# Kernel optimization log

Hardware: AMD Instinct MI355X
Metric: run time of the kernel (lower is better)

Reference implementation:

```python
import jax, jax.numpy as jnp
import numpy as np

B, Q, C = 32, 900, 92
W_CLASS, W_BBOX, W_GIOU = 1.0, 1.0, 1.0
BIG = 100000000.0


def box_cxcywh_to_xyxy(b):
    cx, cy, w, h = b[..., 0], b[..., 1], b[..., 2], b[..., 3]
    return jnp.stack([cx - 0.5 * w, cy - 0.5 * h, cx + 0.5 * w, cy + 0.5 * h], axis=-1)


def pairwise_generalized_box_iou(b1, b2):
    # b1, b2: [B, Q, 4] in xyxy -> [B, Q, Q]
    area1 = (b1[..., 2] - b1[..., 0]) * (b1[..., 3] - b1[..., 1])  # [B,Q]
    area2 = (b2[..., 2] - b2[..., 0]) * (b2[..., 3] - b2[..., 1])  # [B,Q]
    lt = jnp.maximum(b1[:, :, None, :2], b2[:, None, :, :2])  # [B,Q,Q,2]
    rb = jnp.minimum(b1[:, :, None, 2:], b2[:, None, :, 2:])
    wh = jnp.clip(rb - lt, 0.0)
    inter = wh[..., 0] * wh[..., 1]  # [B,Q,Q]
    union = area1[:, :, None] + area2[:, None, :] - inter
    iou = inter / union
    # smallest enclosing box
    lt_e = jnp.minimum(b1[:, :, None, :2], b2[:, None, :, :2])
    rb_e = jnp.maximum(b1[:, :, None, 2:], b2[:, None, :, 2:])
    wh_e = jnp.clip(rb_e - lt_e, 0.0)
    enc = wh_e[..., 0] * wh_e[..., 1]
    return iou - (enc - union) / enc


def setup_inputs() -> dict:
    key = jax.random.key(0)
    k1, k2, k3, k4, k5 = jax.random.split(key, 5)
    return {
        "pred_logits": jax.random.normal(k1, (B, Q, C), dtype=jnp.float32),
        "pred_boxes": jax.random.uniform(k2, (B, Q, 4), dtype=jnp.float32),
        "boxes": jax.random.uniform(k3, (B, Q, 4), dtype=jnp.float32),
        "area": jax.random.uniform(k4, (B, Q), dtype=jnp.float32),
        "labels": jax.random.randint(k5, (B, Q), 0, C),
    }


def reference(pred_logits, pred_boxes, boxes, area, labels):
    b, q, _ = pred_logits.shape
    out_prob = jax.nn.softmax(pred_logits, axis=-1)  # [B,Q,C]
    # cost_class[b,i,j] = -out_prob[b,i,labels[b,j]]
    idx = jnp.broadcast_to(labels[:, None, :], (b, q, q))
    cost_class = -jnp.take_along_axis(out_prob, idx, axis=2)  # [B,Q,Q]
    # pairwise mean-L1 between cxcywh boxes (tf.reduce_mean over last dim)
    cost_bbox = jnp.mean(jnp.abs(pred_boxes[:, :, None, :] - boxes[:, None, :, :]), axis=-1)
    cost_giou = -pairwise_generalized_box_iou(
        box_cxcywh_to_xyxy(pred_boxes), box_cxcywh_to_xyxy(boxes)
    )
    cost = W_BBOX * cost_bbox + W_CLASS * cost_class + W_GIOU * cost_giou
    return jnp.where((area > 0)[:, None, :], cost, BIG)
```

## Files before the change

### kernel.cpp

```cpp
#include <hip/hip_runtime.h>
#include <math.h>

#define Bn  32
#define Qn  900
#define Cn  92
#define TI  12
#define NIT (Qn / TI)
#define NT  (Qn / 4)
#define BLK 256
#define BIGV 100000000.0f

__global__ __launch_bounds__(BLK) void hungarian_cost_kernel(
    const float* __restrict__ logits,
    const float* __restrict__ pboxes,
    const float* __restrict__ gboxes,
    const float* __restrict__ area,
    const int*   __restrict__ labels,
    float* __restrict__ out)
{
    __shared__ float s_x0[Qn], s_y0[Qn], s_x1[Qn], s_y1[Qn];
    __shared__ float s_ab[Qn];
    __shared__ float s_fl[Qn];
    __shared__ int   s_lab[Qn];
    __shared__ float s_prob[TI][Cn];
    __shared__ float4 s_pred[TI];
    __shared__ float  s_predA[TI];

    const int blk = blockIdx.x;
    const int b   = blk / NIT;
    const int i0  = (blk - b * NIT) * TI;
    const int tid = threadIdx.x;

    const float4* gb4 = (const float4*)(gboxes + (size_t)b * Qn * 4);
    const float*  ga  = area   + (size_t)b * Qn;
    const int*    gl  = labels + (size_t)b * Qn;
    for (int j = tid; j < Qn; j += BLK) {
        float4 c = gb4[j];
        s_x0[j] = c.x - 0.5f * c.z;
        s_y0[j] = c.y - 0.5f * c.w;
        s_x1[j] = c.x + 0.5f * c.z;
        s_y1[j] = c.y + 0.5f * c.w;
        s_ab[j] = c.z * c.w;
        s_fl[j] = (ga[j] > 0.0f) ? -3.402823e38f : BIGV;
        s_lab[j] = gl[j];
    }

    {
        const int wave = tid >> 6;
        const int lane = tid & 63;
        for (int rr = wave; rr < TI; rr += 4) {
            const int r = i0 + rr;
            const float* lrow = logits + ((size_t)(b * Qn + r)) * Cn;
            float x0 = lrow[lane];
            float x1 = (lane + 64 < Cn) ? lrow[lane + 64] : -INFINITY;
            float m = fmaxf(x0, x1);
            #pragma unroll
            for (int off = 32; off; off >>= 1)
                m = fmaxf(m, __shfl_xor(m, off));
            float e0 = __expf(x0 - m);
            float e1 = (lane + 64 < Cn) ? __expf(x1 - m) : 0.0f;
            float s = e0 + e1;
            #pragma unroll
            for (int off = 32; off; off >>= 1)
                s += __shfl_xor(s, off);
            float inv = __builtin_amdgcn_rcpf(s);
            s_prob[rr][lane] = e0 * inv;
            if (lane + 64 < Cn) s_prob[rr][lane + 64] = e1 * inv;
            if (lane == 0) {
                float4 c = ((const float4*)(pboxes + (size_t)b * Qn * 4))[r];
                float4 x;
                x.x = c.x - 0.5f * c.z;
                x.y = c.y - 0.5f * c.w;
                x.z = c.x + 0.5f * c.z;
                x.w = c.y + 0.5f * c.w;
                s_pred[rr]  = x;
                s_predA[rr] = c.z * c.w;
            }
        }
    }
    __syncthreads();

    float* obase = out + ((size_t)b * Qn + i0) * Qn;
    for (int f = tid; f < TI * NT; f += BLK) {
        const int il = f / NT;
        const int j4 = (f - il * NT) * 4;

        const float4 P     = s_pred[il];
        const float  areaP = s_predA[il];
        const float* prow  = s_prob[il];

        const float4 X0 = *(const float4*)&s_x0[j4];
        const float4 Y0 = *(const float4*)&s_y0[j4];
        const float4 X1 = *(const float4*)&s_x1[j4];
        const float4 Y1 = *(const float4*)&s_y1[j4];
        const float4 AB = *(const float4*)&s_ab[j4];
        const float4 FL = *(const float4*)&s_fl[j4];
        const int4   LB = *(const int4*)&s_lab[j4];

        auto cost1 = [&](float bx0, float by0, float bx1, float by1,
                         float ab, float fl, int lb) -> float {
            float dx0 = P.x - bx0, dy0 = P.y - by0;
            float dx1 = P.z - bx1, dy1 = P.w - by1;
            float s1 = fabsf(dx0 + dx1) + fabsf(dy0 + dy1);
            float s2 = fabsf(dx1 - dx0) + fabsf(dy1 - dy0);
            float bb = __builtin_fmaf(s1, 0.125f, 0.25f * s2);
            float iw = fminf(P.z, bx1) - fmaxf(P.x, bx0);
            float ih = fminf(P.w, by1) - fmaxf(P.y, by0);
            iw = fmaxf(iw, 0.0f); ih = fmaxf(ih, 0.0f);
            float inter = iw * ih;
            float uni = areaP + ab - inter;
            float ew = fmaxf(P.z, bx1) - fminf(P.x, bx0);
            float eh = fmaxf(P.w, by1) - fminf(P.y, by0);
            float enc = ew * eh;
            float rU = __builtin_amdgcn_rcpf(uni);
            float rE = __builtin_amdgcn_rcpf(enc);
            float g = __builtin_fmaf(inter, rU,
                      __builtin_fmaf(uni, rE, prow[lb] - 1.0f));
            float c = bb - g;
            return fmaxf(c, fl);
        };

        float4 res;
        res.x = cost1(X0.x, Y0.x, X1.x, Y1.x, AB.x, FL.x, LB.x);
        res.y = cost1(X0.y, Y0.y, X1.y, Y1.y, AB.y, FL.y, LB.y);
        res.z = cost1(X0.z, Y0.z, X1.z, Y1.z, AB.z, FL.z, LB.z);
        res.w = cost1(X0.w, Y0.w, X1.w, Y1.w, AB.w, FL.w, LB.w);

        ((float4*)(obase + (size_t)il * Qn))[j4 >> 2] = res;
    }
}

extern "C" void kernel_launch(void* const* d_in, const int* in_sizes, int n_in,
                              void* d_out, int out_size, void* d_ws, size_t ws_size,
                              hipStream_t stream) {
    const float* logits = (const float*)d_in[0];
    const float* pboxes = (const float*)d_in[1];
    const float* gboxes = (const float*)d_in[2];
    const float* areas  = (const float*)d_in[3];
    const int*   labels = (const int*)d_in[4];
    float* out = (float*)d_out;

    hungarian_cost_kernel<<<Bn * NIT, BLK, 0, stream>>>(
        logits, pboxes, gboxes, areas, labels, out);
}
```

Baseline: 45.32 us.

## Keep per-column GT box data in registers and use nontemporal output stores

Each thread now owns a fixed group of 4 target columns. It loads and transforms their boxes, areas and labels once into registers, instead of staging them in shared memory and re-reading them for every row. The per-row loop iterates over the 12 prediction rows with those registers reused, and writes results with nontemporal vector stores to avoid polluting the cache. Only 225 of 256 threads do output work, which slightly lowers lane utilization, and register pressure rises.

```diff
diff --git a/kernel.cpp b/kernel.cpp
--- a/kernel.cpp
+++ b/kernel.cpp
@@ -6,9 +6,12 @@
 #define Cn  92
 #define TI  12
 #define NIT (Qn / TI)
-#define NT  (Qn / 4)
+#define NG  (Qn / 4)
 #define BLK 256
 #define BIGV 100000000.0f
+#define NEGINF -3.402823e38f
+
+typedef float f32x4 __attribute__((ext_vector_type(4)));
 
 __global__ __launch_bounds__(BLK) void hungarian_cost_kernel(
     const float* __restrict__ logits,
@@ -18,11 +21,7 @@
     const int*   __restrict__ labels,
     float* __restrict__ out)
 {
-    __shared__ float s_x0[Qn], s_y0[Qn], s_x1[Qn], s_y1[Qn];
-    __shared__ float s_ab[Qn];
-    __shared__ float s_fl[Qn];
-    __shared__ int   s_lab[Qn];
-    __shared__ float s_prob[TI][Cn];
+    __shared__ float  s_prob[TI][Cn];
     __shared__ float4 s_pred[TI];
     __shared__ float  s_predA[TI];
 
@@ -31,25 +30,35 @@
     const int i0  = (blk - b * NIT) * TI;
     const int tid = threadIdx.x;
 
-    const float4* gb4 = (const float4*)(gboxes + (size_t)b * Qn * 4);
-    const float*  ga  = area   + (size_t)b * Qn;
-    const int*    gl  = labels + (size_t)b * Qn;
-    for (int j = tid; j < Qn; j += BLK) {
-        float4 c = gb4[j];
-        s_x0[j] = c.x - 0.5f * c.z;
-        s_y0[j] = c.y - 0.5f * c.w;
-        s_x1[j] = c.x + 0.5f * c.z;
-        s_y1[j] = c.y + 0.5f * c.w;
-        s_ab[j] = c.z * c.w;
-        s_fl[j] = (ga[j] > 0.0f) ? -3.402823e38f : BIGV;
-        s_lab[j] = gl[j];
+    float X0[4], Y0[4], X1[4], Y1[4], AB[4], FL[4];
+    int   LB[4];
+    if (tid < NG) {
+        const float4* gb4 = (const float4*)(gboxes + (size_t)b * Qn * 4) + tid * 4;
+        const float4  a4  = ((const float4*)(area   + (size_t)b * Qn))[tid];
+        const int4    l4  = ((const int4*)  (labels + (size_t)b * Qn))[tid];
+        #pragma unroll
+        for (int k = 0; k < 4; ++k) {
+            float4 c = gb4[k];
+            X0[k] = c.x - 0.5f * c.z;
+            Y0[k] = c.y - 0.5f * c.w;
+            X1[k] = c.x + 0.5f * c.z;
+            Y1[k] = c.y + 0.5f * c.w;
+            AB[k] = c.z * c.w;
+        }
+        FL[0] = (a4.x > 0.0f) ? NEGINF : BIGV;
+        FL[1] = (a4.y > 0.0f) ? NEGINF : BIGV;
+        FL[2] = (a4.z > 0.0f) ? NEGINF : BIGV;
+        FL[3] = (a4.w > 0.0f) ? NEGINF : BIGV;
+        LB[0] = l4.x; LB[1] = l4.y; LB[2] = l4.z; LB[3] = l4.w;
     }
 
     {
         const int wave = tid >> 6;
         const int lane = tid & 63;
-        for (int rr = wave; rr < TI; rr += 4) {
-            const int r = i0 + rr;
+        #pragma unroll
+        for (int rr0 = 0; rr0 < TI; rr0 += 4) {
+            const int rr = rr0 + wave;
+            const int r  = i0 + rr;
             const float* lrow = logits + ((size_t)(b * Qn + r)) * Cn;
             float x0 = lrow[lane];
             float x1 = (lane + 64 < Cn) ? lrow[lane + 64] : -INFINITY;
@@ -80,53 +89,38 @@
     }
     __syncthreads();
 
-    float* obase = out + ((size_t)b * Qn + i0) * Qn;
-    for (int f = tid; f < TI * NT; f += BLK) {
-        const int il = f / NT;
-        const int j4 = (f - il * NT) * 4;
+    if (tid < NG) {
+        float* obase = out + ((size_t)(b * Qn + i0)) * Qn + tid * 4;
+        for (int il = 0; il < TI; ++il) {
+            const float4 P     = s_pred[il];
+            const float  areaP = s_predA[il];
+            const float* prow  = s_prob[il];
 
-        const float4 P     = s_pred[il];
-        const float  areaP = s_predA[il];
-        const float* prow  = s_prob[il];
-
-        const float4 X0 = *(const float4*)&s_x0[j4];
-        const float4 Y0 = *(const float4*)&s_y0[j4];
-        const float4 X1 = *(const float4*)&s_x1[j4];
-        const float4 Y1 = *(const float4*)&s_y1[j4];
-        const float4 AB = *(const float4*)&s_ab[j4];
-        const float4 FL = *(const float4*)&s_fl[j4];
-        const int4   LB = *(const int4*)&s_lab[j4];
-
-        auto cost1 = [&](float bx0, float by0, float bx1, float by1,
-                         float ab, float fl, int lb) -> float {
-            float dx0 = P.x - bx0, dy0 = P.y - by0;
-            float dx1 = P.z - bx1, dy1 = P.w - by1;
-            float s1 = fabsf(dx0 + dx1) + fabsf(dy0 + dy1);
-            float s2 = fabsf(dx1 - dx0) + fabsf(dy1 - dy0);
-            float bb = __builtin_fmaf(s1, 0.125f, 0.25f * s2);
-            float iw = fminf(P.z, bx1) - fmaxf(P.x, bx0);
-            float ih = fminf(P.w, by1) - fmaxf(P.y, by0);
-            iw = fmaxf(iw, 0.0f); ih = fmaxf(ih, 0.0f);
-            float inter = iw * ih;
-            float uni = areaP + ab - inter;
-            float ew = fmaxf(P.z, bx1) - fminf(P.x, bx0);
-            float eh = fmaxf(P.w, by1) - fminf(P.y, by0);
-            float enc = ew * eh;
-            float rU = __builtin_amdgcn_rcpf(uni);
-            float rE = __builtin_amdgcn_rcpf(enc);
-            float g = __builtin_fmaf(inter, rU,
-                      __builtin_fmaf(uni, rE, prow[lb] - 1.0f));
-            float c = bb - g;
-            return fmaxf(c, fl);
-        };
-
-        float4 res;
-        res.x = cost1(X0.x, Y0.x, X1.x, Y1.x, AB.x, FL.x, LB.x);
-        res.y = cost1(X0.y, Y0.y, X1.y, Y1.y, AB.y, FL.y, LB.y);
-        res.z = cost1(X0.z, Y0.z, X1.z, Y1.z, AB.z, FL.z, LB.z);
-        res.w = cost1(X0.w, Y0.w, X1.w, Y1.w, AB.w, FL.w, LB.w);
-
-        ((float4*)(obase + (size_t)il * Qn))[j4 >> 2] = res;
+            float r[4];
+            #pragma unroll
+            for (int k = 0; k < 4; ++k) {
+                float dx0 = P.x - X0[k], dy0 = P.y - Y0[k];
+                float dx1 = P.z - X1[k], dy1 = P.w - Y1[k];
+                float s1 = fabsf(dx0 + dx1) + fabsf(dy0 + dy1);
+                float s2 = fabsf(dx1 - dx0) + fabsf(dy1 - dy0);
+                float bb = __builtin_fmaf(s1, 0.125f, 0.25f * s2);
+                float iw = fminf(P.z, X1[k]) - fmaxf(P.x, X0[k]);
+                float ih = fminf(P.w, Y1[k]) - fmaxf(P.y, Y0[k]);
+                iw = fmaxf(iw, 0.0f); ih = fmaxf(ih, 0.0f);
+                float inter = iw * ih;
+                float uni = areaP + AB[k] - inter;
+                float ew = fmaxf(P.z, X1[k]) - fminf(P.x, X0[k]);
+                float eh = fmaxf(P.w, Y1[k]) - fminf(P.y, Y0[k]);
+                float enc = ew * eh;
+                float rU = __builtin_amdgcn_rcpf(uni);
+                float rE = __builtin_amdgcn_rcpf(enc);
+                float g = __builtin_fmaf(inter, rU,
+                          __builtin_fmaf(uni, rE, prow[LB[k]] - 1.0f));
+                r[k] = fmaxf(bb - g, FL[k]);
+            }
+            f32x4 res = { r[0], r[1], r[2], r[3] };
+            __builtin_nontemporal_store(res, (f32x4*)(obase + (size_t)il * Qn));
+        }
     }
 }
 
```

After: 43.27 us. 1.05x faster.
